# Performance work log

Measured on AMD Instinct MI355X. Metric: run time of the kernel, lower is better.

The kernel has to match this reference:

```python
import jax, jax.numpy as jnp
import numpy as np

B, T, H, OUT_STEPS, D = 131072, 51, 64, 20, 4


def setup_inputs() -> dict:
    key = jax.random.key(0)
    ks = jax.random.split(key, 11)
    s = 1.0 / np.sqrt(H)  # torch nn.GRU / nn.Linear uniform init bound
    u = lambda k, shape: jax.random.uniform(k, shape, jnp.float32, -s, s)
    return {
        "input_seq": jax.random.normal(ks[0], (B, T, D), jnp.float32),
        "enc_Wih": u(ks[1], (3 * H, D)),
        "enc_Whh": u(ks[2], (3 * H, H)),
        "enc_bih": u(ks[3], (3 * H,)),
        "enc_bhh": u(ks[4], (3 * H,)),
        "dec_Wih": u(ks[5], (3 * H, D)),
        "dec_Whh": u(ks[6], (3 * H, H)),
        "dec_bih": u(ks[7], (3 * H,)),
        "dec_bhh": u(ks[8], (3 * H,)),
        "lin_W": u(ks[9], (D, H)),
        "lin_b": u(ks[10], (D,)),
    }


def _gru_cell(x, h, Wih, Whh, bih, bhh):
    """PyTorch GRU cell semantics. x: [B,D_in], h: [B,H]."""
    gi = x @ Wih.T + bih  # [B,3H]
    gh = h @ Whh.T + bhh  # [B,3H]
    ir, iz, inn = jnp.split(gi, 3, axis=-1)
    hr, hz, hn = jnp.split(gh, 3, axis=-1)
    r = jax.nn.sigmoid(ir + hr)
    z = jax.nn.sigmoid(iz + hz)
    n = jnp.tanh(inn + r * hn)
    return (1.0 - z) * n + z * h


def reference(input_seq, enc_Wih, enc_Whh, enc_bih, enc_bhh,
              dec_Wih, dec_Whh, dec_bih, dec_bhh, lin_W, lin_b):
    # offset: last observed point, broadcast over the 20 output steps
    offset = input_seq[:, -1:, :]  # [B,1,D]
    diffs = input_seq[:, 1:] - input_seq[:, :-1]  # [B,T-1,D]; dropout p=0 -> identity
    h0 = jnp.zeros((input_seq.shape[0], H), input_seq.dtype)

    def enc_step(h, x_t):
        return _gru_cell(x_t, h, enc_Wih, enc_Whh, enc_bih, enc_bhh), None

    hn, _ = jax.lax.scan(enc_step, h0, jnp.swapaxes(diffs, 0, 1))  # final hidden [B,H]

    def dec_step(carry, _):
        h, px = carry
        h = _gru_cell(px, h, dec_Wih, dec_Whh, dec_bih, dec_bhh)
        x = h @ lin_W.T + lin_b + px  # linear + residual
        return (h, x), x

    _, xs = jax.lax.scan(dec_step, (hn, diffs[:, -1]), None, length=OUT_STEPS)
    out = jnp.swapaxes(xs, 0, 1)  # [B,OUT_STEPS,D]
    return out + offset
```

## Files before the change

### kernel.cpp

```cpp
#include <hip/hip_runtime.h>
#include <hip/hip_bf16.h>

namespace {

constexpr int kT = 51;
constexpr int kOut = 20;
constexpr float kL2E  = 1.4426950408889634f;
constexpr float kL2E2 = 2.8853900817779268f;

typedef __attribute__((ext_vector_type(8))) short bf16x8;
typedef __attribute__((ext_vector_type(4))) float f32x4;

union FragU {
    bf16x8 v;
    unsigned long long u64[2];
    unsigned int u32[4];
    unsigned short s[8];
};

__device__ __forceinline__ unsigned short f2bf(float x) {
    union { float f; unsigned int u; } v;
    v.f = x;
    unsigned int r = (v.u + 0x7fffu + ((v.u >> 16) & 1u)) >> 16;
    return (unsigned short)r;
}

__device__ __forceinline__ unsigned int packbf(float a, float b) {
    union { float f; unsigned int u; } ua, ub;
    ua.f = a; ub.f = b;
    return __builtin_amdgcn_perm(ub.u + 0x8000u, ua.u + 0x8000u, 0x07060302u);
}

__global__ __launch_bounds__(256, 3) void gru_encdec(
    const float* __restrict__ input,
    const float* __restrict__ eWih, const float* __restrict__ eWhh,
    const float* __restrict__ ebih, const float* __restrict__ ebhh,
    const float* __restrict__ dWih, const float* __restrict__ dWhh,
    const float* __restrict__ dbih, const float* __restrict__ dbhh,
    const float* __restrict__ linW, const float* __restrict__ linb,
    float* __restrict__ out)
{
    __shared__ __align__(16) unsigned short hbuf[2][2][16 * 68];
    __shared__ __align__(16) float sout[2][16 * 84];

    const int lane = (int)(threadIdx.x & 63u);
    const int w = (int)(threadIdx.x >> 6u);
    const int q = lane >> 4;
    const int i = lane & 15;
    const long b0 = (long)blockIdx.x * 32 + i;
    const float* __restrict__ xrow0 = input + b0 * (kT * 4);
    const float* __restrict__ xrow1 = xrow0 + 16 * (kT * 4);
    const bool q0 = (q == 0);

    bf16x8 WA[3][2];
    bf16x8 WAUG[3];
    f32x4 bhhn4;
    float hp0[4], hp1[4];
    bf16x8 bhA0 = {0,0,0,0,0,0,0,0}, bhB0 = {0,0,0,0,0,0,0,0};
    bf16x8 bhA1 = {0,0,0,0,0,0,0,0}, bhB1 = {0,0,0,0,0,0,0,0};
    float px0[4], px1[4];
    const f32x4 z4 = {0.f, 0.f, 0.f, 0.f};

    auto load_whh = [&](const float* __restrict__ Whh) {
#pragma unroll
        for (int l = 0; l < 3; ++l) {
            const int tau = 4 * l + w;
            const float sc = (l < 2) ? kL2E : kL2E2;
#pragma unroll
            for (int f = 0; f < 2; ++f) {
                const float* ptr = Whh + (tau * 16 + i) * 64 + f * 32 + q * 8;
                FragU fu;
#pragma unroll
                for (int j = 0; j < 8; ++j) fu.s[j] = f2bf(ptr[j] * sc);
                WA[l][f] = fu.v;
            }
        }
    };

    auto load_aug = [&](const float* __restrict__ Wih,
                        const float* __restrict__ bih,
                        const float* __restrict__ bhh) {
#pragma unroll
        for (int l = 0; l < 3; ++l) {
            const int tau = 4 * l + w;
            const float sc = (l < 2) ? kL2E : kL2E2;
            FragU fu;
            fu.u64[0] = 0; fu.u64[1] = 0;
            if (q0) {
                int j = tau * 16 + i;
#pragma unroll
                for (int d = 0; d < 4; ++d) fu.s[d] = f2bf(Wih[j * 4 + d] * sc);
                float bias = (l < 2) ? (bih[j] + bhh[j]) : bih[j];
                fu.s[4] = f2bf(bias * sc);
            }
            WAUG[l] = fu.v;
        }
#pragma unroll
        for (int r = 0; r < 4; ++r)
            bhhn4[r] = bhh[128 + 16 * w + 4 * q + r] * kL2E2;
    };

    auto make_baug = [&](const float* px) -> bf16x8 {
        FragU fu;
        fu.u32[0] = packbf(px[0], px[1]);
        fu.u32[1] = packbf(px[2], px[3]);
        fu.u32[2] = 0x3f80u;
        fu.u32[3] = 0u;
        return fu.v;
    };

    auto gru_step2 = [&](int ssel, bf16x8 ba0, bf16x8 ba1) {
        unsigned short* __restrict__ hw0 = hbuf[ssel][0];
        unsigned short* __restrict__ hw1 = hbuf[ssel][1];
        f32x4 R0 = __builtin_amdgcn_mfma_f32_16x16x32_bf16(WAUG[0], ba0, z4, 0, 0, 0);
        R0 = __builtin_amdgcn_mfma_f32_16x16x32_bf16(WA[0][0], bhA0, R0, 0, 0, 0);
        R0 = __builtin_amdgcn_mfma_f32_16x16x32_bf16(WA[0][1], bhB0, R0, 0, 0, 0);
        f32x4 Z0 = __builtin_amdgcn_mfma_f32_16x16x32_bf16(WAUG[1], ba0, z4, 0, 0, 0);
        Z0 = __builtin_amdgcn_mfma_f32_16x16x32_bf16(WA[1][0], bhA0, Z0, 0, 0, 0);
        Z0 = __builtin_amdgcn_mfma_f32_16x16x32_bf16(WA[1][1], bhB0, Z0, 0, 0, 0);
        f32x4 Ni0 = __builtin_amdgcn_mfma_f32_16x16x32_bf16(WAUG[2], ba0, z4, 0, 0, 0);
        f32x4 Nh0 = __builtin_amdgcn_mfma_f32_16x16x32_bf16(WA[2][0], bhA0, bhhn4, 0, 0, 0);
        Nh0 = __builtin_amdgcn_mfma_f32_16x16x32_bf16(WA[2][1], bhB0, Nh0, 0, 0, 0);
        f32x4 R1 = __builtin_amdgcn_mfma_f32_16x16x32_bf16(WAUG[0], ba1, z4, 0, 0, 0);
        R1 = __builtin_amdgcn_mfma_f32_16x16x32_bf16(WA[0][0], bhA1, R1, 0, 0, 0);
        R1 = __builtin_amdgcn_mfma_f32_16x16x32_bf16(WA[0][1], bhB1, R1, 0, 0, 0);
        f32x4 Z1 = __builtin_amdgcn_mfma_f32_16x16x32_bf16(WAUG[1], ba1, z4, 0, 0, 0);
        Z1 = __builtin_amdgcn_mfma_f32_16x16x32_bf16(WA[1][0], bhA1, Z1, 0, 0, 0);
        Z1 = __builtin_amdgcn_mfma_f32_16x16x32_bf16(WA[1][1], bhB1, Z1, 0, 0, 0);
        f32x4 Ni1 = __builtin_amdgcn_mfma_f32_16x16x32_bf16(WAUG[2], ba1, z4, 0, 0, 0);
        f32x4 Nh1 = __builtin_amdgcn_mfma_f32_16x16x32_bf16(WA[2][0], bhA1, bhhn4, 0, 0, 0);
        Nh1 = __builtin_amdgcn_mfma_f32_16x16x32_bf16(WA[2][1], bhB1, Nh1, 0, 0, 0);

        float hv0[4], hv1[4];
#pragma unroll
        for (int r = 0; r < 4; ++r) {
            float a0 = __builtin_amdgcn_exp2f(-R0[r]);
            float c0 = __builtin_amdgcn_exp2f(-Z0[r]);
            float a1 = __builtin_amdgcn_exp2f(-R1[r]);
            float c1 = __builtin_amdgcn_exp2f(-Z1[r]);
            float A0 = 1.f + a0, C0 = 1.f + c0, P0 = A0 * C0;
            float A1 = 1.f + a1, C1 = 1.f + c1, P1 = A1 * C1;
            float rpp = __builtin_amdgcn_rcpf(P0 * P1);
            float rp0 = rpp * P1, rp1 = rpp * P0;
            float rr0 = rp0 * C0, zz0 = rp0 * A0;
            float rr1 = rp1 * C1, zz1 = rp1 * A1;
            float p20 = __builtin_fmaf(rr0, Nh0[r], Ni0[r]);
            float p21 = __builtin_fmaf(rr1, Nh1[r], Ni1[r]);
            float E0 = __builtin_amdgcn_exp2f(p20);
            float E1 = __builtin_amdgcn_exp2f(p21);
            float D0 = E0 + 1.f, D1 = E1 + 1.f;
            float rdd = __builtin_amdgcn_rcpf(D0 * D1);
            float t0 = rdd * D1, t1 = rdd * D0;
            float n0 = __builtin_fmaf(-2.f, t0, 1.f);
            float n1 = __builtin_fmaf(-2.f, t1, 1.f);
            hv0[r] = __builtin_fmaf(zz0, hp0[r] - n0, n0);
            hv1[r] = __builtin_fmaf(zz1, hp1[r] - n1, n1);
            hp0[r] = hv0[r];
            hp1[r] = hv1[r];
        }
        uint2 wv0, wv1;
        wv0.x = packbf(hv0[0], hv0[1]); wv0.y = packbf(hv0[2], hv0[3]);
        wv1.x = packbf(hv1[0], hv1[1]); wv1.y = packbf(hv1[2], hv1[3]);
        *(uint2*)&hw0[i * 68 + 16 * w + 4 * q] = wv0;
        *(uint2*)&hw1[i * 68 + 16 * w + 4 * q] = wv1;

        __syncthreads();
        FragU f0, f1, g0f, g1f;
        f0.u64[0]  = *(const unsigned long long*)&hw0[i * 68 + 8 * q];
        f0.u64[1]  = *(const unsigned long long*)&hw0[i * 68 + 8 * q + 4];
        f1.u64[0]  = *(const unsigned long long*)&hw0[i * 68 + 32 + 8 * q];
        f1.u64[1]  = *(const unsigned long long*)&hw0[i * 68 + 32 + 8 * q + 4];
        g0f.u64[0] = *(const unsigned long long*)&hw1[i * 68 + 8 * q];
        g0f.u64[1] = *(const unsigned long long*)&hw1[i * 68 + 8 * q + 4];
        g1f.u64[0] = *(const unsigned long long*)&hw1[i * 68 + 32 + 8 * q];
        g1f.u64[1] = *(const unsigned long long*)&hw1[i * 68 + 32 + 8 * q + 4];
        bhA0 = f0.v;  bhB0 = f1.v;
        bhA1 = g0f.v; bhB1 = g1f.v;
    };

#pragma unroll
    for (int r = 0; r < 4; ++r) { hp0[r] = 0.f; hp1[r] = 0.f; }
    load_whh(eWhh);
    load_aug(eWih, ebih, ebhh);

    float4 xp0 = *(const float4*)(xrow0);
    float4 xn0 = *(const float4*)(xrow0 + 4);
    float4 xp1 = *(const float4*)(xrow1);
    float4 xn1 = *(const float4*)(xrow1 + 4);
#pragma unroll 2
    for (int s = 0; s < kT - 1; ++s) {
        int idx = s + 2; if (idx > kT - 1) idx = kT - 1;
        float4 xf0 = *(const float4*)(xrow0 + idx * 4);
        float4 xf1 = *(const float4*)(xrow1 + idx * 4);
        px0[0] = xn0.x - xp0.x; px0[1] = xn0.y - xp0.y;
        px0[2] = xn0.z - xp0.z; px0[3] = xn0.w - xp0.w;
        px1[0] = xn1.x - xp1.x; px1[1] = xn1.y - xp1.y;
        px1[2] = xn1.z - xp1.z; px1[3] = xn1.w - xp1.w;
        gru_step2(s & 1, make_baug(px0), make_baug(px1));
        xp0 = xn0; xn0 = xf0;
        xp1 = xn1; xn1 = xf1;
    }
    float4 off0 = xp0;
    float4 off1 = xp1;

    load_whh(dWhh);
    load_aug(dWih, dbih, dbhh);

    bf16x8 AL0, AL1, AL2;
    {
        FragU a0, a1, a2;
        a0.u64[0] = a0.u64[1] = 0;
        a1.u64[0] = a1.u64[1] = 0;
        a2.u64[0] = a2.u64[1] = 0;
        if (i < 4) {
            const float* p0 = linW + i * 64 + q * 8;
            const float* p1 = linW + i * 64 + 32 + q * 8;
#pragma unroll
            for (int j = 0; j < 8; ++j) {
                a0.s[j] = f2bf(p0[j]);
                a1.s[j] = f2bf(p1[j]);
            }
            if (q0) a2.s[4] = f2bf(linb[i]);
        }
        AL0 = a0.v; AL1 = a1.v; AL2 = a2.v;
    }

#pragma unroll 2
    for (int s = 0; s < kOut; ++s) {
        bf16x8 ba0 = make_baug(px0);
        bf16x8 ba1 = make_baug(px1);
        gru_step2(s & 1, ba0, ba1);
        f32x4 X0 = __builtin_amdgcn_mfma_f32_16x16x32_bf16(AL2, ba0, z4, 0, 0, 0);
        X0 = __builtin_amdgcn_mfma_f32_16x16x32_bf16(AL0, bhA0, X0, 0, 0, 0);
        X0 = __builtin_amdgcn_mfma_f32_16x16x32_bf16(AL1, bhB0, X0, 0, 0, 0);
        f32x4 X1 = __builtin_amdgcn_mfma_f32_16x16x32_bf16(AL2, ba1, z4, 0, 0, 0);
        X1 = __builtin_amdgcn_mfma_f32_16x16x32_bf16(AL0, bhA1, X1, 0, 0, 0);
        X1 = __builtin_amdgcn_mfma_f32_16x16x32_bf16(AL1, bhB1, X1, 0, 0, 0);
        px0[0] += X0[0]; px0[1] += X0[1]; px0[2] += X0[2]; px0[3] += X0[3];
        px1[0] += X1[0]; px1[1] += X1[1]; px1[2] += X1[2]; px1[3] += X1[3];
        if (w == 0 && q0) {
            float* sr = sout[0] + i * 84 + s * 4;
            sr[0] = px0[0] + off0.x; sr[1] = px0[1] + off0.y;
            sr[2] = px0[2] + off0.z; sr[3] = px0[3] + off0.w;
        }
        if (w == 1 && q0) {
            float* sr = sout[1] + i * 84 + s * 4;
            sr[0] = px1[0] + off1.x; sr[1] = px1[1] + off1.y;
            sr[2] = px1[2] + off1.z; sr[3] = px1[3] + off1.w;
        }
    }

    if (w < 2) {
        float* __restrict__ go = out + ((long)blockIdx.x * 32 + w * 16) * (kOut * 4);
        const float* __restrict__ so = sout[w];
#pragma unroll
        for (int it = 0; it < 5; ++it) {
            int g = it * 256 + lane * 4;
            int row = g / 80;
            int e = g - row * 80;
            float4 v = *(const float4*)&so[row * 84 + e];
            *(float4*)&go[g] = v;
        }
    }
}

}

extern "C" void kernel_launch(void* const* d_in, const int* in_sizes, int n_in,
                              void* d_out, int out_size, void* d_ws, size_t ws_size,
                              hipStream_t stream) {
    const float* input = (const float*)d_in[0];
    const float* eWih = (const float*)d_in[1];
    const float* eWhh = (const float*)d_in[2];
    const float* ebih = (const float*)d_in[3];
    const float* ebhh = (const float*)d_in[4];
    const float* dWih = (const float*)d_in[5];
    const float* dWhh = (const float*)d_in[6];
    const float* dbih = (const float*)d_in[7];
    const float* dbhh = (const float*)d_in[8];
    const float* linW = (const float*)d_in[9];
    const float* linb = (const float*)d_in[10];
    float* out = (float*)d_out;

    const int B = in_sizes[0] / (kT * 4);
    const int nblocks = B / 32;
    gru_encdec<<<nblocks, 256, 0, stream>>>(input, eWih, eWhh, ebih, ebhh,
                                            dWih, dWhh, dbih, dbhh,
                                            linW, linb, out);
}
```

Measured before the change: 649.0 us.

## Process four batch groups per block and vectorize gate math with packed float2

Each block now handles 64 sequences (four 16-row groups) instead of 32. That amortizes the per-step __syncthreads and the weight-fragment registers over twice as much MFMA work, and halves the block count. Gate nonlinearities are written with f32x2 vectors so they can lower to packed FP32 ops. Output goes straight to global memory instead of being staged through shared memory. In exchange, register pressure rises and occupancy drops (launch bounds go from 3 to 2 blocks), and the global stores become small and scattered.

```diff
diff --git a/kernel.cpp b/kernel.cpp
--- a/kernel.cpp
+++ b/kernel.cpp
@@ -1,5 +1,4 @@
 #include <hip/hip_runtime.h>
-#include <hip/hip_bf16.h>
 
 namespace {
 
@@ -10,6 +9,7 @@
 
 typedef __attribute__((ext_vector_type(8))) short bf16x8;
 typedef __attribute__((ext_vector_type(4))) float f32x4;
+typedef __attribute__((ext_vector_type(2))) float f32x2;
 
 union FragU {
     bf16x8 v;
@@ -31,7 +31,7 @@
     return __builtin_amdgcn_perm(ub.u + 0x8000u, ua.u + 0x8000u, 0x07060302u);
 }
 
-__global__ __launch_bounds__(256, 3) void gru_encdec(
+__global__ __launch_bounds__(256, 2) void gru_encdec(
     const float* __restrict__ input,
     const float* __restrict__ eWih, const float* __restrict__ eWhh,
     const float* __restrict__ ebih, const float* __restrict__ ebhh,
@@ -40,26 +40,27 @@
     const float* __restrict__ linW, const float* __restrict__ linb,
     float* __restrict__ out)
 {
-    __shared__ __align__(16) unsigned short hbuf[2][2][16 * 68];
-    __shared__ __align__(16) float sout[2][16 * 84];
+    __shared__ __align__(16) unsigned short hbuf[2][4][16 * 68];
 
     const int lane = (int)(threadIdx.x & 63u);
     const int w = (int)(threadIdx.x >> 6u);
     const int q = lane >> 4;
     const int i = lane & 15;
-    const long b0 = (long)blockIdx.x * 32 + i;
-    const float* __restrict__ xrow0 = input + b0 * (kT * 4);
-    const float* __restrict__ xrow1 = xrow0 + 16 * (kT * 4);
     const bool q0 = (q == 0);
+    const long bb = (long)blockIdx.x * 64 + i;
+
+    const float* xrow[4];
+#pragma unroll
+    for (int g = 0; g < 4; ++g) xrow[g] = input + (bb + 16 * g) * (kT * 4);
 
     bf16x8 WA[3][2];
     bf16x8 WAUG[3];
     f32x4 bhhn4;
-    float hp0[4], hp1[4];
-    bf16x8 bhA0 = {0,0,0,0,0,0,0,0}, bhB0 = {0,0,0,0,0,0,0,0};
-    bf16x8 bhA1 = {0,0,0,0,0,0,0,0}, bhB1 = {0,0,0,0,0,0,0,0};
-    float px0[4], px1[4];
+    float hp[4][4];
+    bf16x8 bh[4][2];
+    float px[4][4];
     const f32x4 z4 = {0.f, 0.f, 0.f, 0.f};
+    const bf16x8 zfr = {0, 0, 0, 0, 0, 0, 0, 0};
 
     auto load_whh = [&](const float* __restrict__ Whh) {
 #pragma unroll
@@ -100,108 +101,120 @@
             bhhn4[r] = bhh[128 + 16 * w + 4 * q + r] * kL2E2;
     };
 
-    auto make_baug = [&](const float* px) -> bf16x8 {
+    auto make_baug = [&](const float* pxv) -> bf16x8 {
         FragU fu;
-        fu.u32[0] = packbf(px[0], px[1]);
-        fu.u32[1] = packbf(px[2], px[3]);
+        fu.u32[0] = packbf(pxv[0], pxv[1]);
+        fu.u32[1] = packbf(pxv[2], pxv[3]);
         fu.u32[2] = 0x3f80u;
         fu.u32[3] = 0u;
         return fu.v;
     };
 
-    auto gru_step2 = [&](int ssel, bf16x8 ba0, bf16x8 ba1) {
-        unsigned short* __restrict__ hw0 = hbuf[ssel][0];
-        unsigned short* __restrict__ hw1 = hbuf[ssel][1];
-        f32x4 R0 = __builtin_amdgcn_mfma_f32_16x16x32_bf16(WAUG[0], ba0, z4, 0, 0, 0);
-        R0 = __builtin_amdgcn_mfma_f32_16x16x32_bf16(WA[0][0], bhA0, R0, 0, 0, 0);
-        R0 = __builtin_amdgcn_mfma_f32_16x16x32_bf16(WA[0][1], bhB0, R0, 0, 0, 0);
-        f32x4 Z0 = __builtin_amdgcn_mfma_f32_16x16x32_bf16(WAUG[1], ba0, z4, 0, 0, 0);
-        Z0 = __builtin_amdgcn_mfma_f32_16x16x32_bf16(WA[1][0], bhA0, Z0, 0, 0, 0);
-        Z0 = __builtin_amdgcn_mfma_f32_16x16x32_bf16(WA[1][1], bhB0, Z0, 0, 0, 0);
-        f32x4 Ni0 = __builtin_amdgcn_mfma_f32_16x16x32_bf16(WAUG[2], ba0, z4, 0, 0, 0);
-        f32x4 Nh0 = __builtin_amdgcn_mfma_f32_16x16x32_bf16(WA[2][0], bhA0, bhhn4, 0, 0, 0);
-        Nh0 = __builtin_amdgcn_mfma_f32_16x16x32_bf16(WA[2][1], bhB0, Nh0, 0, 0, 0);
-        f32x4 R1 = __builtin_amdgcn_mfma_f32_16x16x32_bf16(WAUG[0], ba1, z4, 0, 0, 0);
-        R1 = __builtin_amdgcn_mfma_f32_16x16x32_bf16(WA[0][0], bhA1, R1, 0, 0, 0);
-        R1 = __builtin_amdgcn_mfma_f32_16x16x32_bf16(WA[0][1], bhB1, R1, 0, 0, 0);
-        f32x4 Z1 = __builtin_amdgcn_mfma_f32_16x16x32_bf16(WAUG[1], ba1, z4, 0, 0, 0);
-        Z1 = __builtin_amdgcn_mfma_f32_16x16x32_bf16(WA[1][0], bhA1, Z1, 0, 0, 0);
-        Z1 = __builtin_amdgcn_mfma_f32_16x16x32_bf16(WA[1][1], bhB1, Z1, 0, 0, 0);
-        f32x4 Ni1 = __builtin_amdgcn_mfma_f32_16x16x32_bf16(WAUG[2], ba1, z4, 0, 0, 0);
-        f32x4 Nh1 = __builtin_amdgcn_mfma_f32_16x16x32_bf16(WA[2][0], bhA1, bhhn4, 0, 0, 0);
-        Nh1 = __builtin_amdgcn_mfma_f32_16x16x32_bf16(WA[2][1], bhB1, Nh1, 0, 0, 0);
-
-        float hv0[4], hv1[4];
-#pragma unroll
-        for (int r = 0; r < 4; ++r) {
-            float a0 = __builtin_amdgcn_exp2f(-R0[r]);
-            float c0 = __builtin_amdgcn_exp2f(-Z0[r]);
-            float a1 = __builtin_amdgcn_exp2f(-R1[r]);
-            float c1 = __builtin_amdgcn_exp2f(-Z1[r]);
-            float A0 = 1.f + a0, C0 = 1.f + c0, P0 = A0 * C0;
-            float A1 = 1.f + a1, C1 = 1.f + c1, P1 = A1 * C1;
-            float rpp = __builtin_amdgcn_rcpf(P0 * P1);
-            float rp0 = rpp * P1, rp1 = rpp * P0;
-            float rr0 = rp0 * C0, zz0 = rp0 * A0;
-            float rr1 = rp1 * C1, zz1 = rp1 * A1;
-            float p20 = __builtin_fmaf(rr0, Nh0[r], Ni0[r]);
-            float p21 = __builtin_fmaf(rr1, Nh1[r], Ni1[r]);
-            float E0 = __builtin_amdgcn_exp2f(p20);
-            float E1 = __builtin_amdgcn_exp2f(p21);
-            float D0 = E0 + 1.f, D1 = E1 + 1.f;
-            float rdd = __builtin_amdgcn_rcpf(D0 * D1);
-            float t0 = rdd * D1, t1 = rdd * D0;
-            float n0 = __builtin_fmaf(-2.f, t0, 1.f);
-            float n1 = __builtin_fmaf(-2.f, t1, 1.f);
-            hv0[r] = __builtin_fmaf(zz0, hp0[r] - n0, n0);
-            hv1[r] = __builtin_fmaf(zz1, hp1[r] - n1, n1);
-            hp0[r] = hv0[r];
-            hp1[r] = hv1[r];
-        }
-        uint2 wv0, wv1;
-        wv0.x = packbf(hv0[0], hv0[1]); wv0.y = packbf(hv0[2], hv0[3]);
-        wv1.x = packbf(hv1[0], hv1[1]); wv1.y = packbf(hv1[2], hv1[3]);
-        *(uint2*)&hw0[i * 68 + 16 * w + 4 * q] = wv0;
-        *(uint2*)&hw1[i * 68 + 16 * w + 4 * q] = wv1;
-
+    auto gru_step = [&](int ssel, const bf16x8* ba) {
+#pragma unroll
+        for (int p = 0; p < 2; ++p) {
+            const int g0 = 2 * p, g1 = 2 * p + 1;
+            f32x4 R[2], Z[2], Ni[2], Nh[2];
+#pragma unroll
+            for (int k = 0; k < 2; ++k) {
+                const int g = 2 * p + k;
+                R[k] = __builtin_amdgcn_mfma_f32_16x16x32_bf16(WAUG[0], ba[g], z4, 0, 0, 0);
+                R[k] = __builtin_amdgcn_mfma_f32_16x16x32_bf16(WA[0][0], bh[g][0], R[k], 0, 0, 0);
+                R[k] = __builtin_amdgcn_mfma_f32_16x16x32_bf16(WA[0][1], bh[g][1], R[k], 0, 0, 0);
+                Z[k] = __builtin_amdgcn_mfma_f32_16x16x32_bf16(WAUG[1], ba[g], z4, 0, 0, 0);
+                Z[k] = __builtin_amdgcn_mfma_f32_16x16x32_bf16(WA[1][0], bh[g][0], Z[k], 0, 0, 0);
+                Z[k] = __builtin_amdgcn_mfma_f32_16x16x32_bf16(WA[1][1], bh[g][1], Z[k], 0, 0, 0);
+                Ni[k] = __builtin_amdgcn_mfma_f32_16x16x32_bf16(WAUG[2], ba[g], z4, 0, 0, 0);
+                Nh[k] = __builtin_amdgcn_mfma_f32_16x16x32_bf16(WA[2][0], bh[g][0], bhhn4, 0, 0, 0);
+                Nh[k] = __builtin_amdgcn_mfma_f32_16x16x32_bf16(WA[2][1], bh[g][1], Nh[k], 0, 0, 0);
+            }
+            float hva[4], hvb[4];
+            const f32x2 one = {1.f, 1.f};
+            const f32x2 m2 = {-2.f, -2.f};
+#pragma unroll
+            for (int r = 0; r < 4; ++r) {
+                f32x2 a = { __builtin_amdgcn_exp2f(-R[0][r]),
+                            __builtin_amdgcn_exp2f(-R[1][r]) };
+                f32x2 c = { __builtin_amdgcn_exp2f(-Z[0][r]),
+                            __builtin_amdgcn_exp2f(-Z[1][r]) };
+                f32x2 A = a + one, C = c + one;
+                f32x2 P = A * C;
+                float rpp = __builtin_amdgcn_rcpf(P.x * P.y);
+                f32x2 Ps = {P.y, P.x};
+                f32x2 rp = rpp * Ps;
+                f32x2 rr = rp * C;
+                f32x2 zz = rp * A;
+                f32x2 Nh2 = {Nh[0][r], Nh[1][r]};
+                f32x2 Ni2 = {Ni[0][r], Ni[1][r]};
+                f32x2 p2 = __builtin_elementwise_fma(rr, Nh2, Ni2);
+                f32x2 E = { __builtin_amdgcn_exp2f(p2.x),
+                            __builtin_amdgcn_exp2f(p2.y) };
+                f32x2 D = E + one;
+                float rdd = __builtin_amdgcn_rcpf(D.x * D.y);
+                f32x2 Ds = {D.y, D.x};
+                f32x2 t = rdd * Ds;
+                f32x2 n = __builtin_elementwise_fma(t, m2, one);
+                f32x2 h = {hp[g0][r], hp[g1][r]};
+                f32x2 hv = __builtin_elementwise_fma(zz, h - n, n);
+                hp[g0][r] = hv.x; hp[g1][r] = hv.y;
+                hva[r] = hv.x;    hvb[r] = hv.y;
+            }
+            uint2 wva, wvb;
+            wva.x = packbf(hva[0], hva[1]); wva.y = packbf(hva[2], hva[3]);
+            wvb.x = packbf(hvb[0], hvb[1]); wvb.y = packbf(hvb[2], hvb[3]);
+            *(uint2*)&hbuf[ssel][g0][i * 68 + 16 * w + 4 * q] = wva;
+            *(uint2*)&hbuf[ssel][g1][i * 68 + 16 * w + 4 * q] = wvb;
+        }
         __syncthreads();
-        FragU f0, f1, g0f, g1f;
-        f0.u64[0]  = *(const unsigned long long*)&hw0[i * 68 + 8 * q];
-        f0.u64[1]  = *(const unsigned long long*)&hw0[i * 68 + 8 * q + 4];
-        f1.u64[0]  = *(const unsigned long long*)&hw0[i * 68 + 32 + 8 * q];
-        f1.u64[1]  = *(const unsigned long long*)&hw0[i * 68 + 32 + 8 * q + 4];
-        g0f.u64[0] = *(const unsigned long long*)&hw1[i * 68 + 8 * q];
-        g0f.u64[1] = *(const unsigned long long*)&hw1[i * 68 + 8 * q + 4];
-        g1f.u64[0] = *(const unsigned long long*)&hw1[i * 68 + 32 + 8 * q];
-        g1f.u64[1] = *(const unsigned long long*)&hw1[i * 68 + 32 + 8 * q + 4];
-        bhA0 = f0.v;  bhB0 = f1.v;
-        bhA1 = g0f.v; bhB1 = g1f.v;
-    };
-
-#pragma unroll
-    for (int r = 0; r < 4; ++r) { hp0[r] = 0.f; hp1[r] = 0.f; }
+#pragma unroll
+        for (int g = 0; g < 4; ++g) {
+            const unsigned short* hw = hbuf[ssel][g];
+            FragU fA, fB;
+            fA.u64[0] = *(const unsigned long long*)&hw[i * 68 + 8 * q];
+            fA.u64[1] = *(const unsigned long long*)&hw[i * 68 + 8 * q + 4];
+            fB.u64[0] = *(const unsigned long long*)&hw[i * 68 + 32 + 8 * q];
+            fB.u64[1] = *(const unsigned long long*)&hw[i * 68 + 32 + 8 * q + 4];
+            bh[g][0] = fA.v;
+            bh[g][1] = fB.v;
+        }
+    };
+
+#pragma unroll
+    for (int g = 0; g < 4; ++g) {
+#pragma unroll
+        for (int r = 0; r < 4; ++r) hp[g][r] = 0.f;
+        bh[g][0] = zfr;
+        bh[g][1] = zfr;
+    }
     load_whh(eWhh);
     load_aug(eWih, ebih, ebhh);
 
-    float4 xp0 = *(const float4*)(xrow0);
-    float4 xn0 = *(const float4*)(xrow0 + 4);
-    float4 xp1 = *(const float4*)(xrow1);
-    float4 xn1 = *(const float4*)(xrow1 + 4);
+    float4 xp[4], xn[4];
+#pragma unroll
+    for (int g = 0; g < 4; ++g) {
+        xp[g] = *(const float4*)(xrow[g]);
+        xn[g] = *(const float4*)(xrow[g] + 4);
+    }
+    bf16x8 ba[4];
 #pragma unroll 2
     for (int s = 0; s < kT - 1; ++s) {
+#pragma unroll
+        for (int g = 0; g < 4; ++g) {
+            px[g][0] = xn[g].x - xp[g].x; px[g][1] = xn[g].y - xp[g].y;
+            px[g][2] = xn[g].z - xp[g].z; px[g][3] = xn[g].w - xp[g].w;
+            xp[g] = xn[g];
+        }
         int idx = s + 2; if (idx > kT - 1) idx = kT - 1;
-        float4 xf0 = *(const float4*)(xrow0 + idx * 4);
-        float4 xf1 = *(const float4*)(xrow1 + idx * 4);
-        px0[0] = xn0.x - xp0.x; px0[1] = xn0.y - xp0.y;
-        px0[2] = xn0.z - xp0.z; px0[3] = xn0.w - xp0.w;
-        px1[0] = xn1.x - xp1.x; px1[1] = xn1.y - xp1.y;
-        px1[2] = xn1.z - xp1.z; px1[3] = xn1.w - xp1.w;
-        gru_step2(s & 1, make_baug(px0), make_baug(px1));
-        xp0 = xn0; xn0 = xf0;
-        xp1 = xn1; xn1 = xf1;
-    }
-    float4 off0 = xp0;
-    float4 off1 = xp1;
+#pragma unroll
+        for (int g = 0; g < 4; ++g)
+            xn[g] = *(const float4*)(xrow[g] + idx * 4);
+#pragma unroll
+        for (int g = 0; g < 4; ++g) ba[g] = make_baug(px[g]);
+        gru_step(s & 1, ba);
+    }
+    float4 off[4];
+#pragma unroll
+    for (int g = 0; g < 4; ++g) off[g] = xp[g];
 
     load_whh(dWhh);
     load_aug(dWih, dbih, dbhh);
@@ -227,39 +240,26 @@
 
 #pragma unroll 2
     for (int s = 0; s < kOut; ++s) {
-        bf16x8 ba0 = make_baug(px0);
-        bf16x8 ba1 = make_baug(px1);
-        gru_step2(s & 1, ba0, ba1);
-        f32x4 X0 = __builtin_amdgcn_mfma_f32_16x16x32_bf16(AL2, ba0, z4, 0, 0, 0);
-        X0 = __builtin_amdgcn_mfma_f32_16x16x32_bf16(AL0, bhA0, X0, 0, 0, 0);
-        X0 = __builtin_amdgcn_mfma_f32_16x16x32_bf16(AL1, bhB0, X0, 0, 0, 0);
-        f32x4 X1 = __builtin_amdgcn_mfma_f32_16x16x32_bf16(AL2, ba1, z4, 0, 0, 0);
-        X1 = __builtin_amdgcn_mfma_f32_16x16x32_bf16(AL0, bhA1, X1, 0, 0, 0);
-        X1 = __builtin_amdgcn_mfma_f32_16x16x32_bf16(AL1, bhB1, X1, 0, 0, 0);
-        px0[0] += X0[0]; px0[1] += X0[1]; px0[2] += X0[2]; px0[3] += X0[3];
-        px1[0] += X1[0]; px1[1] += X1[1]; px1[2] += X1[2]; px1[3] += X1[3];
-        if (w == 0 && q0) {
-            float* sr = sout[0] + i * 84 + s * 4;
-            sr[0] = px0[0] + off0.x; sr[1] = px0[1] + off0.y;
-            sr[2] = px0[2] + off0.z; sr[3] = px0[3] + off0.w;
-        }
-        if (w == 1 && q0) {
-            float* sr = sout[1] + i * 84 + s * 4;
-            sr[0] = px1[0] + off1.x; sr[1] = px1[1] + off1.y;
-            sr[2] = px1[2] + off1.z; sr[3] = px1[3] + off1.w;
-        }
-    }
-
-    if (w < 2) {
-        float* __restrict__ go = out + ((long)blockIdx.x * 32 + w * 16) * (kOut * 4);
-        const float* __restrict__ so = sout[w];
-#pragma unroll
-        for (int it = 0; it < 5; ++it) {
-            int g = it * 256 + lane * 4;
-            int row = g / 80;
-            int e = g - row * 80;
-            float4 v = *(const float4*)&so[row * 84 + e];
-            *(float4*)&go[g] = v;
+#pragma unroll
+        for (int g = 0; g < 4; ++g) ba[g] = make_baug(px[g]);
+        gru_step(s & 1, ba);
+#pragma unroll
+        for (int g = 0; g < 4; ++g) {
+            f32x4 X = __builtin_amdgcn_mfma_f32_16x16x32_bf16(AL2, ba[g], z4, 0, 0, 0);
+            X = __builtin_amdgcn_mfma_f32_16x16x32_bf16(AL0, bh[g][0], X, 0, 0, 0);
+            X = __builtin_amdgcn_mfma_f32_16x16x32_bf16(AL1, bh[g][1], X, 0, 0, 0);
+            px[g][0] += X[0]; px[g][1] += X[1];
+            px[g][2] += X[2]; px[g][3] += X[3];
+        }
+#pragma unroll
+        for (int g = 0; g < 4; ++g) {
+            if (w == g && q0) {
+                float* op = out + (bb + 16 * g) * (kOut * 4) + s * 4;
+                float4 v;
+                v.x = px[g][0] + off[g].x; v.y = px[g][1] + off[g].y;
+                v.z = px[g][2] + off[g].z; v.w = px[g][3] + off[g].w;
+                *(float4*)op = v;
+            }
         }
     }
 }
@@ -283,7 +283,7 @@
     float* out = (float*)d_out;
 
     const int B = in_sizes[0] / (kT * 4);
-    const int nblocks = B / 32;
+    const int nblocks = B / 64;
     gru_encdec<<<nblocks, 256, 0, stream>>>(input, eWih, eWhh, ebih, ebhh,
                                             dWih, dWhh, dbih, dbhh,
                                             linW, linb, out);
```

Measured after the change: 639.1 us. About the same (-1.5%).
